# Performance work log

Measured on AMD Instinct MI355X. Metric: run time of the kernel, lower is better.

## Reference

```python
import jax, jax.numpy as jnp
import numpy as np

EPS = 1e-6
SIGMA = 1.0       # get_matrix default sigma
INIT_SIGMA = 1.0  # args.init_sigma


def setup_inputs() -> dict:
    key = jax.random.key(0)
    ks = jax.random.split(key, 12)
    B, T, LD, NB = 16, 2048, 256, 32
    s = 1.0 / np.sqrt(LD)
    E_raw = jax.random.normal(ks[5], (LD, LD), jnp.float32)
    E_w, _ = jnp.linalg.qr(E_raw)  # orthogonal like geotorch.orthogonal
    return {
        "Z": jax.random.normal(ks[0], (B, T, LD), jnp.float32),
        "obs_times": jax.random.uniform(ks[1], (B, T, 1), jnp.float32),
        "D": jax.random.normal(ks[2], (NB, LD), jnp.float32),
        "coeff_W": jax.random.normal(ks[3], (NB, LD), jnp.float32) * s,
        "coeff_b": jnp.zeros((NB,), jnp.float32),
        "E_w": E_w.astype(jnp.float32),
        "B_w": jax.random.normal(ks[6], (LD, LD), jnp.float32) * s,
        "C_w": jax.random.normal(ks[7], (LD, LD), jnp.float32) * s,
        "M_w": jax.random.normal(ks[8], (LD, LD), jnp.float32) * s,
        "init_mean_p": jax.random.normal(ks[9], (LD,), jnp.float32),
        "init_log_var": jax.random.normal(ks[10], (LD,), jnp.float32),
        "y_log_var": jax.random.normal(ks[11], (LD,), jnp.float32),
    }


def _binop(qi, qj):
    # (A_j*A_i, Bu_j + A_j*Bu_i): combine earlier element qi with later qj
    A_i, Bu_i = qi
    A_j, Bu_j = qj
    return (A_j * A_i, Bu_j + A_j * Bu_i)


def reference(Z, obs_times, D, coeff_W, coeff_b, E_w, B_w, C_w, M_w,
              init_mean_p, init_log_var, y_log_var):
    LD = Z.shape[-1]
    # alphas = B(Z)
    alphas = jnp.einsum('btd,ed->bte', Z, B_w)                      # (B,T,LD)
    # get_matrix (vectorized over batch and time)
    A_basis = -(jnp.exp(D) + EPS)                                   # (NB,LD), negative
    A_coeff = jax.nn.softmax(jnp.einsum('btd,nd->btn', alphas, coeff_W) + coeff_b, axis=-1)
    A_mat = jnp.einsum('btn,nd->btd', A_coeff, A_basis)             # (B,T,LD)
    exp_A_m = jnp.exp(A_mat * obs_times)                            # mean transition
    exp_B_m = (exp_A_m - 1.0) / A_mat * alphas
    exp_A_v = jnp.exp(2.0 * A_mat * obs_times)                      # var transition
    exp_B_v = 0.5 * SIGMA ** 2 * (exp_A_v - 1.0) / A_mat + EPS
    mats_A = jnp.concatenate([exp_A_m, exp_A_v], axis=-1)           # (B,T,2LD)
    mats_B = jnp.concatenate([exp_B_m, exp_B_v], axis=-1)           # (B,T,2LD)
    # parallel linear-recurrence scan over time
    cum_A, cum_B = jax.lax.associative_scan(_binop, (mats_A, mats_B), axis=1)
    # initial condition in rotated coordinates
    init_mean0 = E_w.T @ init_mean_p                                # (LD,)
    diag_v = INIT_SIGMA * (jnp.exp(init_log_var) + EPS)
    init_var0 = jnp.einsum('ki,k->i', E_w ** 2, diag_v)             # diag(E^T diag(v) E)
    init_mv = jnp.concatenate([init_mean0, init_var0], axis=0)      # (2LD,)
    imv = cum_A * init_mv                                           # (B,T,2LD)
    init_mean, init_var = imv[..., :LD], imv[..., LD:]
    xs_mean, xs_var = cum_B[..., :LD], cum_B[..., LD:]
    y_var = jnp.exp(y_log_var) + EPS
    # output projections: M(E(.)) and history C(E(Z))
    history = jnp.einsum('btd,ed,fe->btf', Z, E_w, C_w)
    means = jnp.einsum('btd,ed,fe->btf', xs_mean + init_mean, E_w, M_w) + history
    stds = jnp.einsum('btd,ed,fe->btf', jnp.sqrt(xs_var + init_var + y_var), E_w, M_w)
    return means, stds, alphas
```

## Files before the change

### kernel.cpp

```cpp
#include <hip/hip_runtime.h>
#include <math.h>

#define EPS 1e-6f

#define B_   16
#define T_   2048
#define LD   256
#define NB   32
#define BT   (B_ * T_)
#define NCH  64
#define CHUNK (T_ / NCH)

typedef short bf16x8 __attribute__((ext_vector_type(8)));
typedef float f32x4  __attribute__((ext_vector_type(4)));

__device__ __forceinline__ unsigned short f2b(float f) {
    unsigned int u = __float_as_uint(f);
    unsigned int r = (u + 0x7fffu + ((u >> 16) & 1u)) >> 16;
    return (unsigned short)r;
}

__device__ __forceinline__ float b2f(unsigned short h) {
    return __uint_as_float(((unsigned int)h) << 16);
}

__device__ __forceinline__ void gl_lds16(const void* g, void* l) {
    __builtin_amdgcn_global_load_lds(
        (const __attribute__((address_space(1))) unsigned int*)g,
        (__attribute__((address_space(3))) unsigned int*)l, 16, 0, 0);
}

__device__ __forceinline__ int xcd_map(int wg) {
    int x = wg & 7, s = wg >> 3;
    return (s & 3) | (x << 2) | ((s >> 2) << 5);
}

__device__ __forceinline__ void stage_tile(const unsigned short* __restrict__ src,
                                           int row0, int stride, int kb,
                                           unsigned short* lds, int wv, int lane) {
#pragma unroll
    for (int cc = 0; cc < 2; ++cc) {
        int c = wv * 2 + cc;
        int r = c * 16 + (lane >> 2);
        int qd = (lane & 3) ^ ((r >> 1) & 3);
        const unsigned short* g = src + (size_t)(row0 + r) * stride + kb + qd * 8;
        gl_lds16(g, lds + c * 512);
    }
}

__device__ __forceinline__ bf16x8 frag_ld(const unsigned short* lds, int row, int qd) {
    int pq = qd ^ ((row >> 1) & 3);
    return *(const bf16x8*)(lds + row * 32 + pq * 8);
}

__device__ __forceinline__ int u_idx(int i, int d) {
    return ((d >> 5) << 10) + (i << 5) + (((((d >> 3) & 3)) ^ (i & 3)) << 3) + (d & 7);
}

__global__ __launch_bounds__(256) void k_pre(const float* __restrict__ Z,
                                             const float* __restrict__ Dm,
                                             const float* __restrict__ cw,
                                             const float* __restrict__ Ew,
                                             const float* __restrict__ Bw,
                                             const float* __restrict__ Cw,
                                             const float* __restrict__ Mw,
                                             const float* __restrict__ imp,
                                             const float* __restrict__ ilv,
                                             const float* __restrict__ ylv,
                                             unsigned short* __restrict__ GMh,
                                             unsigned short* __restrict__ GCh,
                                             unsigned short* __restrict__ cwbh,
                                             float* __restrict__ im0,
                                             float* __restrict__ iv0,
                                             float* __restrict__ yv,
                                             unsigned short* __restrict__ AbTh,
                                             unsigned short* __restrict__ AbTl,
                                             unsigned short* __restrict__ Bwh,
                                             unsigned short* __restrict__ Zh) {
    int bid = blockIdx.x;
    int tid = threadIdx.x;
    if (bid < 544) {
        const float* W; const float* E; unsigned short* out; int d0, f0;
        if (bid < 256)      { W = Mw; E = Ew; out = GMh;  d0 = (bid & 15) * 16; f0 = (bid >> 4) * 16; }
        else if (bid < 512) { W = Cw; E = Ew; out = GCh;  d0 = (bid & 15) * 16; f0 = ((bid - 256) >> 4) * 16; }
        else                { W = cw; E = Bw; out = cwbh; d0 = (bid & 15) * 16; f0 = ((bid - 512) >> 4) * 16; }
        __shared__ float Ws[16][17];
        __shared__ float Es[16][17];
        int tx = tid & 15, ty = tid >> 4;
        float acc = 0.f;
        for (int eb = 0; eb < LD; eb += 16) {
            Ws[ty][tx] = W[(f0 + ty) * LD + eb + tx];
            Es[ty][tx] = E[(eb + ty) * LD + d0 + tx];
            __syncthreads();
#pragma unroll
            for (int k = 0; k < 16; ++k) acc = fmaf(Ws[ty][k], Es[k][tx], acc);
            __syncthreads();
        }
        out[(f0 + ty) * LD + d0 + tx] = f2b(acc);
    } else if (bid < 577) {
        int sub = bid - 544;
        int t = tid;
        if (sub == 0) {
            float sm = 0.f, sv = 0.f;
            for (int k = 0; k < LD; ++k) {
                float e = Ew[k * LD + t];
                sm = fmaf(e, imp[k], sm);
                sv = fmaf(e * e, expf(ilv[k]) + EPS, sv);
            }
            im0[t] = sm;
            iv0[t] = sv;
            yv[t]  = expf(ylv[t]) + EPS;
        } else {
            int n = sub - 1;
            float a = -(expf(Dm[n * LD + t]) + EPS);
            unsigned short h = f2b(a);
            AbTh[t * NB + n] = h;
            AbTl[t * NB + n] = f2b(a - b2f(h));
        }
    } else if (bid < 641) {
        int i = (bid - 577) * 256 + tid;
        float4 v = ((const float4*)Bw)[i];
        ((ushort4*)Bwh)[i] = make_ushort4(f2b(v.x), f2b(v.y), f2b(v.z), f2b(v.w));
    } else {
        int i = (bid - 641) * 256 + tid;
        float4 v = ((const float4*)Z)[i];
        ((ushort4*)Zh)[i] = make_ushort4(f2b(v.x), f2b(v.y), f2b(v.z), f2b(v.w));
    }
}

__global__ __launch_bounds__(256) void k_zb(const unsigned short* __restrict__ Zh,
                                            const unsigned short* __restrict__ Bwh,
                                            const unsigned short* __restrict__ cwbh,
                                            const float* __restrict__ cb,
                                            float* __restrict__ alphas,
                                            float* __restrict__ logits) {
    __shared__ unsigned short As[128 * 32];
    __shared__ unsigned short Bs[128 * 32];
    int tid = threadIdx.x, lane = tid & 63, wv = tid >> 6;
    int m0 = blockIdx.x * 128;
    int y  = blockIdx.y;
    if (y < 2) {
        int n0 = y * 128;
        int wm = (wv & 1) * 64, wn = (wv >> 1) * 64;
        f32x4 acc[4][4];
#pragma unroll
        for (int i = 0; i < 4; ++i)
#pragma unroll
            for (int j = 0; j < 4; ++j) acc[i][j] = (f32x4){0.f, 0.f, 0.f, 0.f};
        for (int kb = 0; kb < LD; kb += 32) {
            stage_tile(Zh, m0, LD, kb, As, wv, lane);
            stage_tile(Bwh, n0, LD, kb, Bs, wv, lane);
            __syncthreads();
            int qd = lane >> 4;
            bf16x8 af[4], bf[4];
#pragma unroll
            for (int i = 0; i < 4; ++i) af[i] = frag_ld(As, wm + i * 16 + (lane & 15), qd);
#pragma unroll
            for (int j = 0; j < 4; ++j) bf[j] = frag_ld(Bs, wn + j * 16 + (lane & 15), qd);
#pragma unroll
            for (int i = 0; i < 4; ++i)
#pragma unroll
                for (int j = 0; j < 4; ++j)
                    acc[i][j] = __builtin_amdgcn_mfma_f32_16x16x32_bf16(af[i], bf[j], acc[i][j], 0, 0, 0);
            __syncthreads();
        }
        int col = wn + (lane & 15);
        int rb  = wm + ((lane >> 4) << 2);
#pragma unroll
        for (int i = 0; i < 4; ++i)
#pragma unroll
            for (int j = 0; j < 4; ++j)
#pragma unroll
                for (int r = 0; r < 4; ++r)
                    alphas[(size_t)(m0 + rb + i * 16 + r) * LD + n0 + col + j * 16] = acc[i][j][r];
    } else {
        f32x4 acc[2][2];
#pragma unroll
        for (int i = 0; i < 2; ++i)
#pragma unroll
            for (int j = 0; j < 2; ++j) acc[i][j] = (f32x4){0.f, 0.f, 0.f, 0.f};
        for (int kb = 0; kb < LD; kb += 32) {
            stage_tile(Zh, m0, LD, kb, As, wv, lane);
            if (wv < 2) {
                int r = wv * 16 + (lane >> 2);
                int qd = (lane & 3) ^ ((r >> 1) & 3);
                gl_lds16(cwbh + (size_t)r * LD + kb + qd * 8, Bs + wv * 512);
            }
            __syncthreads();
            int qd = lane >> 4;
            bf16x8 af[2], bff[2];
#pragma unroll
            for (int i = 0; i < 2; ++i) af[i] = frag_ld(As, wv * 32 + i * 16 + (lane & 15), qd);
#pragma unroll
            for (int j = 0; j < 2; ++j) bff[j] = frag_ld(Bs, j * 16 + (lane & 15), qd);
#pragma unroll
            for (int i = 0; i < 2; ++i)
#pragma unroll
                for (int j = 0; j < 2; ++j)
                    acc[i][j] = __builtin_amdgcn_mfma_f32_16x16x32_bf16(af[i], bff[j], acc[i][j], 0, 0, 0);
            __syncthreads();
        }
        int col = lane & 15;
        int rb  = (lane >> 4) << 2;
#pragma unroll
        for (int i = 0; i < 2; ++i)
#pragma unroll
            for (int j = 0; j < 2; ++j)
#pragma unroll
                for (int r = 0; r < 4; ++r) {
                    int row = m0 + wv * 32 + i * 16 + rb + r;
                    int cc  = j * 16 + col;
                    logits[(size_t)row * NB + cc] = acc[i][j][r] + cb[cc];
                }
    }
}

__global__ __launch_bounds__(256) void k_tot(const float* __restrict__ logits,
                                             const float* __restrict__ alphas,
                                             const float* __restrict__ obs,
                                             const unsigned short* __restrict__ AbTh,
                                             const unsigned short* __restrict__ AbTl,
                                             float* __restrict__ totA,
                                             float* __restrict__ totBm,
                                             float* __restrict__ totBv) {
    __shared__ unsigned int U[8192];
    __shared__ unsigned short Ph[1024];
    __shared__ unsigned short Pl[1024];
    int tid = threadIdx.x;
    int d = tid;
    int bid = xcd_map(blockIdx.x);
    int bt0 = bid * CHUNK;

    float av[32];
#pragma unroll
    for (int i = 0; i < 32; ++i) av[i] = alphas[(size_t)(bt0 + i) * LD + d];

    int l = tid & 31, rg = tid >> 5;
#pragma unroll
    for (int jj = 0; jj < 4; ++jj) {
        int row = rg * 4 + jj;
        float v = logits[(size_t)(bt0 + row) * NB + l];
        float mx = v;
#pragma unroll
        for (int off = 16; off >= 1; off >>= 1) mx = fmaxf(mx, __shfl_xor(mx, off, 32));
        float e = __expf(v - mx);
        float s = e;
#pragma unroll
        for (int off = 16; off >= 1; off >>= 1) s += __shfl_xor(s, off, 32);
        float p = e * __builtin_amdgcn_rcpf(s);
        unsigned short h = f2b(p);
        unsigned short lo = f2b(p - b2f(h));
        int sa = row * 32 + ((((l >> 3) ^ ((row >> 1) & 3))) << 3) + (l & 7);
        Ph[sa] = h;
        Pl[sa] = lo;
    }
    __syncthreads();

    int lane = tid & 63, wv = tid >> 6;
    int qd = lane >> 4, mr = lane & 15;
    bf16x8 ph[2], pl[2];
#pragma unroll
    for (int iT = 0; iT < 2; ++iT) {
        ph[iT] = frag_ld(Ph, iT * 16 + mr, qd);
        pl[iT] = frag_ld(Pl, iT * 16 + mr, qd);
    }
#pragma unroll
    for (int j = 0; j < 4; ++j) {
        int dcol = wv * 64 + j * 16 + mr;
        bf16x8 ah = *(const bf16x8*)(AbTh + dcol * NB + qd * 8);
        bf16x8 al = *(const bf16x8*)(AbTl + dcol * NB + qd * 8);
#pragma unroll
        for (int iT = 0; iT < 2; ++iT) {
            f32x4 acc = (f32x4){0.f, 0.f, 0.f, 0.f};
            acc = __builtin_amdgcn_mfma_f32_16x16x32_bf16(ph[iT], ah, acc, 0, 0, 0);
            acc = __builtin_amdgcn_mfma_f32_16x16x32_bf16(pl[iT], ah, acc, 0, 0, 0);
            acc = __builtin_amdgcn_mfma_f32_16x16x32_bf16(ph[iT], al, acc, 0, 0, 0);
#pragma unroll
            for (int r = 0; r < 4; ++r)
                U[u_idx(iT * 16 + qd * 4 + r, dcol)] = __float_as_uint(acc[r]);
        }
    }
    __syncthreads();

    float ra = 1.f, rm = 0.f, rv = 0.f;
    int ubase = ((d >> 5) << 10) + (d & 7);
    int qb = (d >> 3) & 3;
#pragma unroll
    for (int i = 0; i < CHUNK; ++i) {
        int ui = ubase + (i << 5) + ((qb ^ (i & 3)) << 3);
        float Am = __uint_as_float(U[ui]);
        float tt = obs[bt0 + i];
        float eAm = __expf(Am * tt);
        float ieA = __builtin_amdgcn_rcpf(Am);
        float e2  = eAm * eAm;
        float eBm = (eAm - 1.f) * ieA * av[i];
        float eBv = fmaf(0.5f * (e2 - 1.f), ieA, EPS);
        rm = fmaf(eAm, rm, eBm);
        rv = fmaf(e2, rv, eBv);
        ra *= eAm;
    }
    int pidx = bid * LD + d;
    totA[pidx] = ra; totBm[pidx] = rm; totBv[pidx] = rv;
}

__global__ __launch_bounds__(256) void k_chunkpfx(const float* __restrict__ totA,
                                                  const float* __restrict__ totBm,
                                                  const float* __restrict__ totBv,
                                                  float* __restrict__ preA,
                                                  float* __restrict__ preBm,
                                                  float* __restrict__ preBv) {
    int d = threadIdx.x;
    int b = blockIdx.x;
    float Pa = 1.f, Pm = 0.f, Pv = 0.f;
    for (int g = 0; g < 8; ++g) {
        float a8[8], m8[8], v8[8];
#pragma unroll
        for (int k = 0; k < 8; ++k) {
            int pidx = (b * NCH + g * 8 + k) * LD + d;
            a8[k] = totA[pidx]; m8[k] = totBm[pidx]; v8[k] = totBv[pidx];
        }
#pragma unroll
        for (int k = 0; k < 8; ++k) {
            int pidx = (b * NCH + g * 8 + k) * LD + d;
            preA[pidx] = Pa; preBm[pidx] = Pm; preBv[pidx] = Pv;
            Pm = fmaf(a8[k], Pm, m8[k]);
            Pv = fmaf(a8[k] * a8[k], Pv, v8[k]);
            Pa *= a8[k];
        }
    }
}

__global__ __launch_bounds__(256) void k_sms(const float* __restrict__ logits,
                                             const float* __restrict__ alphas,
                                             const float* __restrict__ obs,
                                             const unsigned short* __restrict__ AbTh,
                                             const unsigned short* __restrict__ AbTl,
                                             const float* __restrict__ preA,
                                             const float* __restrict__ preBm,
                                             const float* __restrict__ preBv,
                                             const float* __restrict__ im0,
                                             const float* __restrict__ iv0,
                                             const float* __restrict__ yv,
                                             const unsigned short* __restrict__ Zh,
                                             const unsigned short* __restrict__ GMh,
                                             const unsigned short* __restrict__ GCh,
                                             float* __restrict__ means,
                                             float* __restrict__ stds) {
    __shared__ unsigned int U[8192];
    __shared__ unsigned short Ph[1024];
    __shared__ unsigned short Pl[1024];
    __shared__ float obs_s[CHUNK];
    int tid = threadIdx.x, lane = tid & 63, wv = tid >> 6;
    int d = tid;
    int bt0 = blockIdx.x * CHUNK;

    if (tid < CHUNK) obs_s[tid] = obs[bt0 + tid];
    int l = tid & 31, rg = tid >> 5;
#pragma unroll
    for (int jj = 0; jj < 4; ++jj) {
        int row = rg * 4 + jj;
        float v = logits[(size_t)(bt0 + row) * NB + l];
        float mx = v;
#pragma unroll
        for (int off = 16; off >= 1; off >>= 1) mx = fmaxf(mx, __shfl_xor(mx, off, 32));
        float e = __expf(v - mx);
        float s = e;
#pragma unroll
        for (int off = 16; off >= 1; off >>= 1) s += __shfl_xor(s, off, 32);
        float p = e * __builtin_amdgcn_rcpf(s);
        unsigned short h = f2b(p);
        unsigned short lo = f2b(p - b2f(h));
        int sa = row * 32 + ((((l >> 3) ^ ((row >> 1) & 3))) << 3) + (l & 7);
        Ph[sa] = h;
        Pl[sa] = lo;
    }
    __syncthreads();

    int qd = lane >> 4, mr = lane & 15;
    bf16x8 ph[2], pl[2];
#pragma unroll
    for (int iT = 0; iT < 2; ++iT) {
        ph[iT] = frag_ld(Ph, iT * 16 + mr, qd);
        pl[iT] = frag_ld(Pl, iT * 16 + mr, qd);
    }
#pragma unroll
    for (int j = 0; j < 4; ++j) {
        int dcol = wv * 64 + j * 16 + mr;
        bf16x8 ah = *(const bf16x8*)(AbTh + dcol * NB + qd * 8);
        bf16x8 al = *(const bf16x8*)(AbTl + dcol * NB + qd * 8);
#pragma unroll
        for (int iT = 0; iT < 2; ++iT) {
            f32x4 acc = (f32x4){0.f, 0.f, 0.f, 0.f};
            acc = __builtin_amdgcn_mfma_f32_16x16x32_bf16(ph[iT], ah, acc, 0, 0, 0);
            acc = __builtin_amdgcn_mfma_f32_16x16x32_bf16(pl[iT], ah, acc, 0, 0, 0);
            acc = __builtin_amdgcn_mfma_f32_16x16x32_bf16(ph[iT], al, acc, 0, 0, 0);
#pragma unroll
            for (int r = 0; r < 4; ++r)
                U[u_idx(iT * 16 + qd * 4 + r, dcol)] = __float_as_uint(acc[r]);
        }
    }
    __syncthreads();

    int pidx = blockIdx.x * LD + d;
    float ga = preA[pidx], gm = preBm[pidx], gv = preBv[pidx];
    float i0 = im0[d], v0 = iv0[d], yvd = yv[d];

    int ubase = ((d >> 5) << 10) + (d & 7);
    int qb = (d >> 3) & 3;
    for (int g = 0; g < 4; ++g) {
        float av[8];
#pragma unroll
        for (int k = 0; k < 8; ++k)
            av[k] = alphas[(size_t)(bt0 + g * 8 + k) * LD + d];
#pragma unroll
        for (int k = 0; k < 8; ++k) {
            int i = g * 8 + k;
            int ui = ubase + (i << 5) + ((qb ^ (i & 3)) << 3);
            float Am = __uint_as_float(U[ui]);
            float tt = obs_s[i];
            float eAm = __expf(Am * tt);
            float ieA = __builtin_amdgcn_rcpf(Am);
            float e2  = eAm * eAm;
            float eBm = (eAm - 1.f) * ieA * av[k];
            float eBv = fmaf(0.5f * (e2 - 1.f), ieA, EPS);
            gm = fmaf(eAm, gm, eBm);
            gv = fmaf(e2, gv, eBv);
            ga *= eAm;
            float mm = fmaf(ga, i0, gm);
            float vv = fmaf(ga * ga, v0, gv) + yvd;
            float ss = sqrtf(vv);
            U[ui] = ((unsigned int)f2b(mm) << 16) | (unsigned int)f2b(ss);
        }
    }
    __syncthreads();

    f32x4 accm[2][4], accs[2][4];
#pragma unroll
    for (int iT = 0; iT < 2; ++iT)
#pragma unroll
        for (int j = 0; j < 4; ++j) {
            accm[iT][j] = (f32x4){0.f, 0.f, 0.f, 0.f};
            accs[iT][j] = (f32x4){0.f, 0.f, 0.f, 0.f};
        }
    for (int kc = 0; kc < 8; ++kc) {
        bf16x8 am[2], asv[2], az[2];
#pragma unroll
        for (int iT = 0; iT < 2; ++iT) {
            int row = iT * 16 + mr;
            int off = (kc << 10) + (row << 5) + ((qd ^ (row & 3)) << 3);
            uint4 ua = *(const uint4*)(U + off);
            uint4 ub = *(const uint4*)(U + off + 4);
            unsigned int uu[8] = {ua.x, ua.y, ua.z, ua.w, ub.x, ub.y, ub.z, ub.w};
            bf16x8 m_, s_;
#pragma unroll
            for (int k = 0; k < 8; ++k) {
                m_[k] = (short)(uu[k] >> 16);
                s_[k] = (short)(uu[k] & 0xffffu);
            }
            am[iT] = m_; asv[iT] = s_;
            az[iT] = *(const bf16x8*)(Zh + (size_t)(bt0 + row) * LD + kc * 32 + qd * 8);
        }
#pragma unroll
        for (int j = 0; j < 4; ++j) {
            int brow = wv * 64 + j * 16 + mr;
            bf16x8 bm = *(const bf16x8*)(GMh + (size_t)brow * LD + kc * 32 + qd * 8);
            bf16x8 bc = *(const bf16x8*)(GCh + (size_t)brow * LD + kc * 32 + qd * 8);
#pragma unroll
            for (int iT = 0; iT < 2; ++iT) {
                accm[iT][j] = __builtin_amdgcn_mfma_f32_16x16x32_bf16(am[iT],  bm, accm[iT][j], 0, 0, 0);
                accs[iT][j] = __builtin_amdgcn_mfma_f32_16x16x32_bf16(asv[iT], bm, accs[iT][j], 0, 0, 0);
                accm[iT][j] = __builtin_amdgcn_mfma_f32_16x16x32_bf16(az[iT],  bc, accm[iT][j], 0, 0, 0);
            }
        }
    }

    int col0 = wv * 64 + mr;
    int rb   = (lane >> 4) << 2;
#pragma unroll
    for (int i = 0; i < 2; ++i)
#pragma unroll
        for (int j = 0; j < 4; ++j)
#pragma unroll
            for (int r = 0; r < 4; ++r) {
                size_t off = (size_t)(bt0 + i * 16 + rb + r) * LD + col0 + j * 16;
                means[off] = accm[i][j][r];
                stds[off]  = accs[i][j][r];
            }
}

extern "C" void kernel_launch(void* const* d_in, const int* in_sizes, int n_in,
                              void* d_out, int out_size, void* d_ws, size_t ws_size,
                              hipStream_t stream) {
    const float* Z   = (const float*)d_in[0];
    const float* obs = (const float*)d_in[1];
    const float* Dm  = (const float*)d_in[2];
    const float* cw  = (const float*)d_in[3];
    const float* cb  = (const float*)d_in[4];
    const float* Ew  = (const float*)d_in[5];
    const float* Bw  = (const float*)d_in[6];
    const float* Cw  = (const float*)d_in[7];
    const float* Mw  = (const float*)d_in[8];
    const float* imp = (const float*)d_in[9];
    const float* ilv = (const float*)d_in[10];
    const float* ylv = (const float*)d_in[11];

    float* out    = (float*)d_out;
    float* means  = out;
    float* stds   = out + (size_t)BT * LD;
    float* alphas = out + (size_t)2 * BT * LD;

    char* ws = (char*)d_ws;
    size_t o = 0;
    unsigned short* Zh   = (unsigned short*)(ws + o); o += (size_t)BT * LD * 2;
    float*          logits=(float*)(ws + o);          o += (size_t)BT * NB * 4;
    unsigned short* GMh  = (unsigned short*)(ws + o); o += (size_t)LD * LD * 2;
    unsigned short* GCh  = (unsigned short*)(ws + o); o += (size_t)LD * LD * 2;
    unsigned short* Bwh  = (unsigned short*)(ws + o); o += (size_t)LD * LD * 2;
    unsigned short* cwbh = (unsigned short*)(ws + o); o += (size_t)NB * LD * 2;
    unsigned short* AbTh = (unsigned short*)(ws + o); o += (size_t)LD * NB * 2;
    unsigned short* AbTl = (unsigned short*)(ws + o); o += (size_t)LD * NB * 2;
    float* totA  = (float*)(ws + o); o += (size_t)B_ * NCH * LD * 4;
    float* totBm = (float*)(ws + o); o += (size_t)B_ * NCH * LD * 4;
    float* totBv = (float*)(ws + o); o += (size_t)B_ * NCH * LD * 4;
    float* preA  = (float*)(ws + o); o += (size_t)B_ * NCH * LD * 4;
    float* preBm = (float*)(ws + o); o += (size_t)B_ * NCH * LD * 4;
    float* preBv = (float*)(ws + o); o += (size_t)B_ * NCH * LD * 4;
    float* im0   = (float*)(ws + o); o += LD * 4;
    float* iv0   = (float*)(ws + o); o += LD * 4;
    float* yv    = (float*)(ws + o); o += LD * 4;

    k_pre<<<dim3(641 + BT * LD / 1024), dim3(256), 0, stream>>>(
        Z, Dm, cw, Ew, Bw, Cw, Mw, imp, ilv, ylv,
        GMh, GCh, cwbh, im0, iv0, yv, AbTh, AbTl, Bwh, Zh);

    k_zb<<<dim3(BT / 128, 3), dim3(256), 0, stream>>>(Zh, Bwh, cwbh, cb, alphas, logits);

    k_tot<<<dim3(B_ * NCH), dim3(256), 0, stream>>>(logits, alphas, obs, AbTh, AbTl,
                                                    totA, totBm, totBv);
    k_chunkpfx<<<dim3(B_), dim3(LD), 0, stream>>>(totA, totBm, totBv, preA, preBm, preBv);

    k_sms<<<dim3(B_ * NCH), dim3(256), 0, stream>>>(logits, alphas, obs, AbTh, AbTl,
                                                    preA, preBm, preBv,
                                                    im0, iv0, yv,
                                                    Zh, GMh, GCh, means, stds);
}
```

Baseline: 235.6 us.

## Process two scan chunks per block in k_sms to reuse weight fragments

Each k_sms block now handles 64 time rows (two chunks) instead of 32, halving the grid. The two chunks' recurrences are interleaved for ILP, and the GM/GC/AbT weight fragments loaded from global memory are reused across twice as many rows in the MFMA loops. The P staging buffers are aliased into a doubled U shared buffer, and obs is read directly from global memory instead of being staged in LDS. In exchange, LDS use rises to 64KB and the accumulator count doubles, which lowers occupancy and leaves only 512 blocks.

```diff
diff --git a/kernel.cpp b/kernel.cpp
--- a/kernel.cpp
+++ b/kernel.cpp
@@ -346,19 +346,17 @@
                                              const unsigned short* __restrict__ GCh,
                                              float* __restrict__ means,
                                              float* __restrict__ stds) {
-    __shared__ unsigned int U[8192];
-    __shared__ unsigned short Ph[1024];
-    __shared__ unsigned short Pl[1024];
-    __shared__ float obs_s[CHUNK];
+    __shared__ unsigned int U[16384];
+    unsigned short* Ph = (unsigned short*)U;
+    unsigned short* Pl = (unsigned short*)(U + 1024);
     int tid = threadIdx.x, lane = tid & 63, wv = tid >> 6;
     int d = tid;
-    int bt0 = blockIdx.x * CHUNK;
-
-    if (tid < CHUNK) obs_s[tid] = obs[bt0 + tid];
+    int bt0 = blockIdx.x * 64;
+
     int l = tid & 31, rg = tid >> 5;
 #pragma unroll
-    for (int jj = 0; jj < 4; ++jj) {
-        int row = rg * 4 + jj;
+    for (int jj = 0; jj < 8; ++jj) {
+        int row = rg * 8 + jj;
         float v = logits[(size_t)(bt0 + row) * NB + l];
         float mx = v;
 #pragma unroll
@@ -377,77 +375,96 @@
     __syncthreads();
 
     int qd = lane >> 4, mr = lane & 15;
-    bf16x8 ph[2], pl[2];
-#pragma unroll
-    for (int iT = 0; iT < 2; ++iT) {
+    bf16x8 ph[4], pl[4];
+#pragma unroll
+    for (int iT = 0; iT < 4; ++iT) {
         ph[iT] = frag_ld(Ph, iT * 16 + mr, qd);
         pl[iT] = frag_ld(Pl, iT * 16 + mr, qd);
     }
+    __syncthreads();
+
 #pragma unroll
     for (int j = 0; j < 4; ++j) {
         int dcol = wv * 64 + j * 16 + mr;
         bf16x8 ah = *(const bf16x8*)(AbTh + dcol * NB + qd * 8);
         bf16x8 al = *(const bf16x8*)(AbTl + dcol * NB + qd * 8);
 #pragma unroll
-        for (int iT = 0; iT < 2; ++iT) {
+        for (int iT = 0; iT < 4; ++iT) {
             f32x4 acc = (f32x4){0.f, 0.f, 0.f, 0.f};
             acc = __builtin_amdgcn_mfma_f32_16x16x32_bf16(ph[iT], ah, acc, 0, 0, 0);
             acc = __builtin_amdgcn_mfma_f32_16x16x32_bf16(pl[iT], ah, acc, 0, 0, 0);
             acc = __builtin_amdgcn_mfma_f32_16x16x32_bf16(ph[iT], al, acc, 0, 0, 0);
 #pragma unroll
-            for (int r = 0; r < 4; ++r)
-                U[u_idx(iT * 16 + qd * 4 + r, dcol)] = __float_as_uint(acc[r]);
+            for (int r = 0; r < 4; ++r) {
+                int i = iT * 16 + qd * 4 + r;
+                U[((i >> 5) << 13) + u_idx(i & 31, dcol)] = __float_as_uint(acc[r]);
+            }
         }
     }
     __syncthreads();
 
-    int pidx = blockIdx.x * LD + d;
-    float ga = preA[pidx], gm = preBm[pidx], gv = preBv[pidx];
+    int p0 = (blockIdx.x * 2) * LD + d;
+    float ga0 = preA[p0],      gm0 = preBm[p0],      gv0 = preBv[p0];
+    float ga1 = preA[p0 + LD], gm1 = preBm[p0 + LD], gv1 = preBv[p0 + LD];
     float i0 = im0[d], v0 = iv0[d], yvd = yv[d];
 
     int ubase = ((d >> 5) << 10) + (d & 7);
     int qb = (d >> 3) & 3;
     for (int g = 0; g < 4; ++g) {
-        float av[8];
-#pragma unroll
-        for (int k = 0; k < 8; ++k)
-            av[k] = alphas[(size_t)(bt0 + g * 8 + k) * LD + d];
+        float av0[8], av1[8];
+#pragma unroll
+        for (int k = 0; k < 8; ++k) {
+            av0[k] = alphas[(size_t)(bt0 + g * 8 + k) * LD + d];
+            av1[k] = alphas[(size_t)(bt0 + 32 + g * 8 + k) * LD + d];
+        }
 #pragma unroll
         for (int k = 0; k < 8; ++k) {
             int i = g * 8 + k;
-            int ui = ubase + (i << 5) + ((qb ^ (i & 3)) << 3);
-            float Am = __uint_as_float(U[ui]);
-            float tt = obs_s[i];
-            float eAm = __expf(Am * tt);
-            float ieA = __builtin_amdgcn_rcpf(Am);
-            float e2  = eAm * eAm;
-            float eBm = (eAm - 1.f) * ieA * av[k];
-            float eBv = fmaf(0.5f * (e2 - 1.f), ieA, EPS);
-            gm = fmaf(eAm, gm, eBm);
-            gv = fmaf(e2, gv, eBv);
-            ga *= eAm;
-            float mm = fmaf(ga, i0, gm);
-            float vv = fmaf(ga * ga, v0, gv) + yvd;
-            float ss = sqrtf(vv);
-            U[ui] = ((unsigned int)f2b(mm) << 16) | (unsigned int)f2b(ss);
+            int ui0 = ubase + (i << 5) + ((qb ^ (i & 3)) << 3);
+            int ui1 = 8192 + ui0;
+            float Am0 = __uint_as_float(U[ui0]);
+            float Am1 = __uint_as_float(U[ui1]);
+            float t0 = obs[bt0 + i];
+            float t1 = obs[bt0 + 32 + i];
+            float e0 = __expf(Am0 * t0);
+            float e1 = __expf(Am1 * t1);
+            float r0 = __builtin_amdgcn_rcpf(Am0);
+            float r1 = __builtin_amdgcn_rcpf(Am1);
+            float q0 = e0 * e0, q1 = e1 * e1;
+            float bm0 = (e0 - 1.f) * r0 * av0[k];
+            float bm1 = (e1 - 1.f) * r1 * av1[k];
+            float bv0 = fmaf(0.5f * (q0 - 1.f), r0, EPS);
+            float bv1 = fmaf(0.5f * (q1 - 1.f), r1, EPS);
+            gm0 = fmaf(e0, gm0, bm0);   gm1 = fmaf(e1, gm1, bm1);
+            gv0 = fmaf(q0, gv0, bv0);   gv1 = fmaf(q1, gv1, bv1);
+            ga0 *= e0;                  ga1 *= e1;
+            float mm0 = fmaf(ga0, i0, gm0);
+            float mm1 = fmaf(ga1, i0, gm1);
+            float vv0 = fmaf(ga0 * ga0, v0, gv0) + yvd;
+            float vv1 = fmaf(ga1 * ga1, v0, gv1) + yvd;
+            float ss0 = sqrtf(vv0);
+            float ss1 = sqrtf(vv1);
+            U[ui0] = ((unsigned int)f2b(mm0) << 16) | (unsigned int)f2b(ss0);
+            U[ui1] = ((unsigned int)f2b(mm1) << 16) | (unsigned int)f2b(ss1);
         }
     }
     __syncthreads();
 
-    f32x4 accm[2][4], accs[2][4];
-#pragma unroll
-    for (int iT = 0; iT < 2; ++iT)
+    f32x4 accm[4][4], accs[4][4];
+#pragma unroll
+    for (int iT = 0; iT < 4; ++iT)
 #pragma unroll
         for (int j = 0; j < 4; ++j) {
             accm[iT][j] = (f32x4){0.f, 0.f, 0.f, 0.f};
             accs[iT][j] = (f32x4){0.f, 0.f, 0.f, 0.f};
         }
     for (int kc = 0; kc < 8; ++kc) {
-        bf16x8 am[2], asv[2], az[2];
-#pragma unroll
-        for (int iT = 0; iT < 2; ++iT) {
+        bf16x8 am[4], asv[4], az[4];
+#pragma unroll
+        for (int iT = 0; iT < 4; ++iT) {
             int row = iT * 16 + mr;
-            int off = (kc << 10) + (row << 5) + ((qd ^ (row & 3)) << 3);
+            int ii = row & 31;
+            int off = ((row >> 5) << 13) + (kc << 10) + (ii << 5) + ((qd ^ (ii & 3)) << 3);
             uint4 ua = *(const uint4*)(U + off);
             uint4 ub = *(const uint4*)(U + off + 4);
             unsigned int uu[8] = {ua.x, ua.y, ua.z, ua.w, ub.x, ub.y, ub.z, ub.w};
@@ -466,7 +483,7 @@
             bf16x8 bm = *(const bf16x8*)(GMh + (size_t)brow * LD + kc * 32 + qd * 8);
             bf16x8 bc = *(const bf16x8*)(GCh + (size_t)brow * LD + kc * 32 + qd * 8);
 #pragma unroll
-            for (int iT = 0; iT < 2; ++iT) {
+            for (int iT = 0; iT < 4; ++iT) {
                 accm[iT][j] = __builtin_amdgcn_mfma_f32_16x16x32_bf16(am[iT],  bm, accm[iT][j], 0, 0, 0);
                 accs[iT][j] = __builtin_amdgcn_mfma_f32_16x16x32_bf16(asv[iT], bm, accs[iT][j], 0, 0, 0);
                 accm[iT][j] = __builtin_amdgcn_mfma_f32_16x16x32_bf16(az[iT],  bc, accm[iT][j], 0, 0, 0);
@@ -477,14 +494,14 @@
     int col0 = wv * 64 + mr;
     int rb   = (lane >> 4) << 2;
 #pragma unroll
-    for (int i = 0; i < 2; ++i)
+    for (int iT = 0; iT < 4; ++iT)
 #pragma unroll
         for (int j = 0; j < 4; ++j)
 #pragma unroll
             for (int r = 0; r < 4; ++r) {
-                size_t off = (size_t)(bt0 + i * 16 + rb + r) * LD + col0 + j * 16;
-                means[off] = accm[i][j][r];
-                stds[off]  = accs[i][j][r];
+                size_t off = (size_t)(bt0 + iT * 16 + rb + r) * LD + col0 + j * 16;
+                means[off] = accm[iT][j][r];
+                stds[off]  = accs[iT][j][r];
             }
 }
 
@@ -539,8 +556,8 @@
                                                     totA, totBm, totBv);
     k_chunkpfx<<<dim3(B_), dim3(LD), 0, stream>>>(totA, totBm, totBv, preA, preBm, preBv);
 
-    k_sms<<<dim3(B_ * NCH), dim3(256), 0, stream>>>(logits, alphas, obs, AbTh, AbTl,
-                                                    preA, preBm, preBv,
-                                                    im0, iv0, yv,
-                                                    Zh, GMh, GCh, means, stds);
-}
+    k_sms<<<dim3(B_ * NCH / 2), dim3(256), 0, stream>>>(logits, alphas, obs, AbTh, AbTl,
+                                                        preA, preBm, preBv,
+                                                        im0, iv0, yv,
+                                                        Zh, GMh, GCh, means, stds);
+}
```

New measurement: 234.5 us. Within noise of the previous version (-0.5%).
